# Optimization experiments

Measured on AMD Instinct MI355X. Metric: run time of the kernel, lower is better.

Reference implementation:

```python
import jax, jax.numpy as jnp
import numpy as np

BS = 128          # block_size for weight scales
FP8_MAX = 448.0   # e4m3fn max


def setup_inputs() -> dict:
    key = jax.random.key(0)
    k1, k2, k3 = jax.random.split(key, 3)
    T, I, O = 8192, 4096, 6144  # tokens, input_size, output_size
    x = jax.random.normal(k1, (T, I), dtype=jnp.float32)
    # weight is stored as fp8 in the module; we generate fp32 and cast inside reference
    weight = jax.random.normal(k2, (O, I), dtype=jnp.float32) * 0.02
    weight_scale_inv = jax.random.uniform(k3, (O // BS, I // BS), dtype=jnp.float32,
                                          minval=0.5, maxval=1.5)
    return {"x": x, "weight": weight, "weight_scale_inv": weight_scale_inv}


def reference(x, weight, weight_scale_inv):
    # --- stored fp8 weight (module keeps weight in float8_e4m3fn) ---
    w_fp8 = weight.astype(jnp.float8_e4m3fn)
    O, I = w_fp8.shape
    # --- block-wise dequantization: W_deq[o,i] = w[o,i] * scale[o//BS, i//BS] ---
    w_deq = (w_fp8.astype(jnp.float32)
             .reshape(O // BS, BS, I // BS, BS)
             * weight_scale_inv[:, None, :, None]).reshape(O, I)
    # --- dynamic per-token fp8 quantization of activations ---
    amax = jnp.clip(jnp.max(jnp.abs(x), axis=-1, keepdims=True), 1e-12, None)
    x_scale = (amax / FP8_MAX).astype(jnp.float32)   # [T, 1]
    x_fp8 = (x / x_scale).astype(jnp.float8_e4m3fn)  # [T, I]
    # --- GEMM on dequantized operands: out = (x_fp8 * x_scale) @ W_deq^T ---
    out = (x_fp8.astype(jnp.float32) @ w_deq.T) * x_scale  # [T, O]
    return out
```

## Files before the change

kernel.cpp:

```cpp
#include <hip/hip_runtime.h>
#include <hip/hip_bf16.h>
#include <stdint.h>

#define T_TOK 8192
#define K_IN  4096
#define O_OUT 6144

typedef __attribute__((ext_vector_type(4))) float f32x4;
typedef __attribute__((ext_vector_type(8))) int i32x8;
typedef unsigned int uint32;


__device__ inline void load_lds_16(const void* g, void* l) {
    __builtin_amdgcn_global_load_lds(
        (const __attribute__((address_space(1))) unsigned int*)g,
        (__attribute__((address_space(3))) unsigned int*)l, 16, 0, 0);
}

__device__ inline int pack4_fp8(float a, float b, float c, float d) {
    int r = __builtin_amdgcn_cvt_pk_fp8_f32(a, b, 0, false);
    r = __builtin_amdgcn_cvt_pk_fp8_f32(c, d, r, true);
    return r;
}

__global__ __launch_bounds__(256) void quant_x(const float* __restrict__ x,
                                               uint32* __restrict__ xq,
                                               float* __restrict__ xscale) {
    const int t   = blockIdx.x;
    const int tid = threadIdx.x;
    const float4* row4 = (const float4*)(x + (size_t)t * K_IN);

    float4 v[4];
    float amax = 0.f;
#pragma unroll
    for (int j = 0; j < 4; ++j) {
        v[j] = row4[tid + j * 256];
        amax = fmaxf(amax, fmaxf(fmaxf(fabsf(v[j].x), fabsf(v[j].y)),
                                 fmaxf(fabsf(v[j].z), fabsf(v[j].w))));
    }
#pragma unroll
    for (int off = 32; off > 0; off >>= 1)
        amax = fmaxf(amax, __shfl_down(amax, off, 64));
    __shared__ float red[4];
    if ((tid & 63) == 0) red[tid >> 6] = amax;
    __syncthreads();
    amax = fmaxf(fmaxf(red[0], red[1]), fmaxf(red[2], red[3]));

    const float scale = fmaxf(amax, 1e-12f) / 448.0f;
    if (tid == 0) xscale[t] = scale;

    uint32* orow = xq + (size_t)t * (K_IN / 4);
#pragma unroll
    for (int j = 0; j < 4; ++j) {
        float q0 = v[j].x / scale, q1 = v[j].y / scale;
        float q2 = v[j].z / scale, q3 = v[j].w / scale;
        orow[tid + j * 256] = (uint32)pack4_fp8(q0, q1, q2, q3);
    }
}

__global__ __launch_bounds__(256) void quant_w(const float* __restrict__ w,
                                               uint32* __restrict__ wq) {
    const size_t u = (size_t)blockIdx.x * 256 + threadIdx.x;
    float4 v = ((const float4*)w)[u];
    wq[u] = (uint32)pack4_fp8(v.x, v.y, v.z, v.w);
}

__global__ __launch_bounds__(256) void gemm_fp8(const unsigned char* __restrict__ A,
                                                const unsigned char* __restrict__ B,
                                                const float* __restrict__ sinv,
                                                const float* __restrict__ xscale,
                                                float* __restrict__ C) {
    constexpr int BM = 128, BN = 128, BK = 128;
    __shared__ unsigned char As[BM * BK];
    __shared__ unsigned char Bs[BN * BK];

    const int bn = blockIdx.x;
    const int bm = blockIdx.y;
    const int tid  = threadIdx.x;
    const int lane = tid & 63;
    const int wv   = tid >> 6;
    const int wm   = (wv >> 1) * 64;
    const int wn   = (wv & 1) * 64;

    const unsigned char* Abase = A + (size_t)(bm * BM) * K_IN;
    const unsigned char* Bbase = B + (size_t)(bn * BN) * K_IN;
    const float* srow = sinv + bn * (K_IN / 128);

    f32x4 acc[4][4] = {};
    float s_prev = srow[0];

    for (int kb = 0; kb < K_IN / BK; ++kb) {
        const int k0 = kb * BK;
#pragma unroll
        for (int s = 0; s < 4; ++s) {
            int c  = s * 256 + tid;
            int r  = c >> 3;
            int kc = (c & 7) ^ (r & 7);
            load_lds_16(Abase + (size_t)r * K_IN + k0 + kc * 16, &As[c * 16]);
        }
#pragma unroll
        for (int s = 0; s < 4; ++s) {
            int c  = s * 256 + tid;
            int r  = c >> 3;
            int kc = (c & 7) ^ (r & 7);
            load_lds_16(Bbase + (size_t)r * K_IN + k0 + kc * 16, &Bs[c * 16]);
        }
        __syncthreads();

        const float s_cur = srow[kb];
        const float rr = s_prev / s_cur;
        s_prev = s_cur;
#pragma unroll
        for (int i = 0; i < 4; ++i)
#pragma unroll
            for (int j = 0; j < 4; ++j)
                acc[i][j] = acc[i][j] * rr;

        union F { i32x8 v; int4 h[2]; } a[4], b[4];
        const int G2 = (lane >> 4) * 2;
#pragma unroll
        for (int i = 0; i < 4; ++i) {
            int r = wm + i * 16 + (lane & 15);
            a[i].h[0] = *(const int4*)&As[(r * 8 + (G2 ^ (r & 7))) * 16];
            a[i].h[1] = *(const int4*)&As[(r * 8 + ((G2 + 1) ^ (r & 7))) * 16];
        }
#pragma unroll
        for (int j = 0; j < 4; ++j) {
            int r = wn + j * 16 + (lane & 15);
            b[j].h[0] = *(const int4*)&Bs[(r * 8 + (G2 ^ (r & 7))) * 16];
            b[j].h[1] = *(const int4*)&Bs[(r * 8 + ((G2 + 1) ^ (r & 7))) * 16];
        }

#pragma unroll
        for (int i = 0; i < 4; ++i)
#pragma unroll
            for (int j = 0; j < 4; ++j)
                acc[i][j] = __builtin_amdgcn_mfma_scale_f32_16x16x128_f8f6f4(
                    a[i].v, b[j].v, acc[i][j],
                    0 , 0 ,
                    0, 0x7f7f7f7f,
                    0, 0x7f7f7f7f);
        __syncthreads();
    }

#pragma unroll
    for (int i = 0; i < 4; ++i) {
#pragma unroll
        for (int r = 0; r < 4; ++r) {
            int m_g = bm * BM + wm + i * 16 + (lane >> 4) * 4 + r;
            float f = xscale[m_g] * s_prev;
            float* crow = C + (size_t)m_g * O_OUT + bn * BN + wn;
#pragma unroll
            for (int j = 0; j < 4; ++j)
                crow[j * 16 + (lane & 15)] = acc[i][j][r] * f;
        }
    }
}

extern "C" void kernel_launch(void* const* d_in, const int* in_sizes, int n_in,
                              void* d_out, int out_size, void* d_ws, size_t ws_size,
                              hipStream_t stream) {
    const float* x    = (const float*)d_in[0];
    const float* w    = (const float*)d_in[1];
    const float* sinv = (const float*)d_in[2];
    float* out = (float*)d_out;

    char* ws = (char*)d_ws;
    uint32* xq = (uint32*)ws;
    uint32* wq = (uint32*)(ws + (size_t)T_TOK * K_IN);
    float* xscale = (float*)(ws + (size_t)T_TOK * K_IN
                                + (size_t)O_OUT * K_IN);

    quant_x<<<T_TOK, 256, 0, stream>>>(x, xq, xscale);
    quant_w<<<(O_OUT * K_IN) / (4 * 256), 256, 0, stream>>>(w, wq);
    dim3 grid(O_OUT / 128, T_TOK / 128);
    gemm_fp8<<<grid, 256, 0, stream>>>((const unsigned char*)xq,
                                       (const unsigned char*)wq,
                                       sinv, xscale, out);
}
```

Measured before the change: 639.9 us.

## Use 256x256 double-buffered LDS tiles with phased MFMA/load interleave

Rewrites the FP8 GEMM to use 256x256 output tiles with 512 threads (8 waves, each computing a 128x64 sub-tile), so each block does more math per byte loaded. It double-buffers the 128-byte K slices in 128KB of dynamic LDS, issuing the next tile's global-to-LDS copies while the current tile is computed. The MFMA work is split into four phases bracketed by barriers and s_setprio, so LDS fragment reads and accumulator rescaling interleave with matrix ops. The costs are heavy LDS use (one block per CU), many accumulator registers, and extra barriers inside each K step.

```diff
diff --git a/kernel.cpp b/kernel.cpp
--- a/kernel.cpp
+++ b/kernel.cpp
@@ -1,5 +1,4 @@
 #include <hip/hip_runtime.h>
-#include <hip/hip_bf16.h>
 #include <stdint.h>
 
 #define T_TOK 8192
@@ -65,96 +64,143 @@
     wq[u] = (uint32)pack4_fp8(v.x, v.y, v.z, v.w);
 }
 
-__global__ __launch_bounds__(256) void gemm_fp8(const unsigned char* __restrict__ A,
-                                                const unsigned char* __restrict__ B,
-                                                const float* __restrict__ sinv,
-                                                const float* __restrict__ xscale,
-                                                float* __restrict__ C) {
-    constexpr int BM = 128, BN = 128, BK = 128;
-    __shared__ unsigned char As[BM * BK];
-    __shared__ unsigned char Bs[BN * BK];
-
-    const int bn = blockIdx.x;
-    const int bm = blockIdx.y;
-    const int tid  = threadIdx.x;
+__global__ __launch_bounds__(512, 2) void gemm_fp8(const unsigned char* __restrict__ A,
+                                                   const unsigned char* __restrict__ B,
+                                                   const float* __restrict__ sinv,
+                                                   const float* __restrict__ xscale,
+                                                   float* __restrict__ C) {
+    constexpr int BM = 256, BN = 256, BK = 128;
+    constexpr int NKB = K_IN / BK;
+    extern __shared__ unsigned char smem[];
+
+    const int bn  = blockIdx.x;
+    const int bm  = blockIdx.y;
+    const int tid = threadIdx.x;
     const int lane = tid & 63;
     const int wv   = tid >> 6;
-    const int wm   = (wv >> 1) * 64;
-    const int wn   = (wv & 1) * 64;
-
-    const unsigned char* Abase = A + (size_t)(bm * BM) * K_IN;
-    const unsigned char* Bbase = B + (size_t)(bn * BN) * K_IN;
-    const float* srow = sinv + bn * (K_IN / 128);
-
-    f32x4 acc[4][4] = {};
+    const int wm   = (wv >> 2) * 128;
+    const int wn   = (wv & 3) * 64;
+    const int G2   = (lane >> 4) * 2;
+
+    const int tr = tid >> 3;
+    const int kc = (tid & 7) ^ (tr & 7);
+    const unsigned char* Ag = A + (size_t)(bm * BM + tr) * K_IN + kc * 16;
+    const unsigned char* Bg = B + (size_t)(bn * BN + tr) * K_IN + kc * 16;
+    const int ldst = tid * 16;
+
+    const int rA  = lane & 15;
+    const int sw  = lane & 7;
+    const int cs0 = ((G2    ) ^ sw) * 16;
+    const int cs1 = ((G2 | 1) ^ sw) * 16;
+
+    const float* srow = sinv + (size_t)(bn * 2 + (wn >> 7)) * NKB;
+
+    f32x4 acc[8][4] = {};
     float s_prev = srow[0];
 
-    for (int kb = 0; kb < K_IN / BK; ++kb) {
-        const int k0 = kb * BK;
-#pragma unroll
-        for (int s = 0; s < 4; ++s) {
-            int c  = s * 256 + tid;
-            int r  = c >> 3;
-            int kc = (c & 7) ^ (r & 7);
-            load_lds_16(Abase + (size_t)r * K_IN + k0 + kc * 16, &As[c * 16]);
-        }
-#pragma unroll
-        for (int s = 0; s < 4; ++s) {
-            int c  = s * 256 + tid;
-            int r  = c >> 3;
-            int kc = (c & 7) ^ (r & 7);
-            load_lds_16(Bbase + (size_t)r * K_IN + k0 + kc * 16, &Bs[c * 16]);
-        }
-        __syncthreads();
-
+#define STAGE_A(p_, k0_) {                                                   \
+    unsigned char* d_ = smem + (p_) * 65536 + ldst;                          \
+    _Pragma("unroll")                                                        \
+    for (int s_ = 0; s_ < 4; ++s_)                                           \
+        load_lds_16(Ag + (size_t)(s_ * 64) * K_IN + (k0_), d_ + s_ * 8192); }
+#define STAGE_B(p_, k0_) {                                                   \
+    unsigned char* d_ = smem + (p_) * 65536 + 32768 + ldst;                  \
+    _Pragma("unroll")                                                        \
+    for (int s_ = 0; s_ < 4; ++s_)                                           \
+        load_lds_16(Bg + (size_t)(s_ * 64) * K_IN + (k0_), d_ + s_ * 8192); }
+
+    union F { i32x8 v; int4 h[2]; };
+    F a[4], b01[2], b23[2];
+
+#define LDA(d_, i_) { const unsigned char* q_ = pA + (wm + (i_) * 16 + rA) * 128; \
+    (d_).h[0] = *(const int4*)(q_ + cs0); (d_).h[1] = *(const int4*)(q_ + cs1); }
+#define LDB(d_, j_) { const unsigned char* q_ = pB + (wn + (j_) * 16 + rA) * 128; \
+    (d_).h[0] = *(const int4*)(q_ + cs0); (d_).h[1] = *(const int4*)(q_ + cs1); }
+#define MFMA(i_, j_, af_, bf_)                                              \
+    acc[i_][j_] = __builtin_amdgcn_mfma_scale_f32_16x16x128_f8f6f4(         \
+        (af_).v, (bf_).v, acc[i_][j_], 0 , 0 ,            \
+        0, 0x7f7f7f7f, 0, 0x7f7f7f7f);
+#define WAIT_MFMA_PHASE() do {                                              \
+    asm volatile("" ::: "memory");                                          \
+    __builtin_amdgcn_s_barrier();                                           \
+    asm volatile("s_waitcnt lgkmcnt(0)" ::: "memory");                      \
+    __builtin_amdgcn_sched_barrier(0);                                      \
+    __builtin_amdgcn_s_setprio(1); } while (0)
+#define END_MFMA_PHASE() do {                                               \
+    __builtin_amdgcn_s_setprio(0);                                          \
+    asm volatile("" ::: "memory");                                          \
+    __builtin_amdgcn_s_barrier();                                           \
+    asm volatile("" ::: "memory"); } while (0)
+
+    STAGE_A(0, 0); STAGE_B(0, 0);
+    __syncthreads();
+
+    for (int kb = 0; kb < NKB; ++kb) {
+        const unsigned char* pA = smem + (kb & 1) * 65536;
+        const unsigned char* pB = pA + 32768;
+        const int  pn  = (kb & 1) ^ 1;
+        const int  nk0 = (kb + 1) * BK;
+        const bool pf  = (kb + 1) < NKB;
         const float s_cur = srow[kb];
         const float rr = s_prev / s_cur;
         s_prev = s_cur;
-#pragma unroll
-        for (int i = 0; i < 4; ++i)
-#pragma unroll
-            for (int j = 0; j < 4; ++j)
-                acc[i][j] = acc[i][j] * rr;
-
-        union F { i32x8 v; int4 h[2]; } a[4], b[4];
-        const int G2 = (lane >> 4) * 2;
-#pragma unroll
-        for (int i = 0; i < 4; ++i) {
-            int r = wm + i * 16 + (lane & 15);
-            a[i].h[0] = *(const int4*)&As[(r * 8 + (G2 ^ (r & 7))) * 16];
-            a[i].h[1] = *(const int4*)&As[(r * 8 + ((G2 + 1) ^ (r & 7))) * 16];
-        }
-#pragma unroll
-        for (int j = 0; j < 4; ++j) {
-            int r = wn + j * 16 + (lane & 15);
-            b[j].h[0] = *(const int4*)&Bs[(r * 8 + (G2 ^ (r & 7))) * 16];
-            b[j].h[1] = *(const int4*)&Bs[(r * 8 + ((G2 + 1) ^ (r & 7))) * 16];
-        }
-
-#pragma unroll
-        for (int i = 0; i < 4; ++i)
-#pragma unroll
-            for (int j = 0; j < 4; ++j)
-                acc[i][j] = __builtin_amdgcn_mfma_scale_f32_16x16x128_f8f6f4(
-                    a[i].v, b[j].v, acc[i][j],
-                    0 , 0 ,
-                    0, 0x7f7f7f7f,
-                    0, 0x7f7f7f7f);
+
+        if (pf) STAGE_A(pn, nk0);
+        LDA(a[0], 0) LDA(a[1], 1) LDA(a[2], 2) LDA(a[3], 3)
+        LDB(b01[0], 0) LDB(b01[1], 1)
+#pragma unroll
+        for (int i = 0; i < 4; ++i) { acc[i][0] *= rr; acc[i][1] *= rr; }
+        WAIT_MFMA_PHASE();
+#pragma unroll
+        for (int i = 0; i < 4; ++i) { MFMA(i, 0, a[i], b01[0]); MFMA(i, 1, a[i], b01[1]); }
+        END_MFMA_PHASE();
+
+        if (pf) STAGE_B(pn, nk0);
+        LDB(b23[0], 2) LDB(b23[1], 3)
+#pragma unroll
+        for (int i = 0; i < 4; ++i) { acc[i][2] *= rr; acc[i][3] *= rr; }
+        WAIT_MFMA_PHASE();
+#pragma unroll
+        for (int i = 0; i < 4; ++i) { MFMA(i, 2, a[i], b23[0]); MFMA(i, 3, a[i], b23[1]); }
+        END_MFMA_PHASE();
+
+        LDA(a[0], 4) LDA(a[1], 5) LDA(a[2], 6) LDA(a[3], 7)
+#pragma unroll
+        for (int i = 0; i < 4; ++i) { acc[4 + i][2] *= rr; acc[4 + i][3] *= rr; }
+        WAIT_MFMA_PHASE();
+#pragma unroll
+        for (int i = 0; i < 4; ++i) { MFMA(4 + i, 2, a[i], b23[0]); MFMA(4 + i, 3, a[i], b23[1]); }
+        END_MFMA_PHASE();
+
+        LDB(b01[0], 0) LDB(b01[1], 1)
+#pragma unroll
+        for (int i = 0; i < 4; ++i) { acc[4 + i][0] *= rr; acc[4 + i][1] *= rr; }
+        WAIT_MFMA_PHASE();
+#pragma unroll
+        for (int i = 0; i < 4; ++i) { MFMA(4 + i, 0, a[i], b01[0]); MFMA(4 + i, 1, a[i], b01[1]); }
+        __builtin_amdgcn_s_setprio(0);
         __syncthreads();
     }
 
 #pragma unroll
-    for (int i = 0; i < 4; ++i) {
+    for (int i = 0; i < 8; ++i) {
 #pragma unroll
         for (int r = 0; r < 4; ++r) {
-            int m_g = bm * BM + wm + i * 16 + (lane >> 4) * 4 + r;
-            float f = xscale[m_g] * s_prev;
+            const int m_g = bm * BM + wm + i * 16 + (lane >> 4) * 4 + r;
+            const float f = xscale[m_g] * s_prev;
             float* crow = C + (size_t)m_g * O_OUT + bn * BN + wn;
 #pragma unroll
             for (int j = 0; j < 4; ++j)
                 crow[j * 16 + (lane & 15)] = acc[i][j][r] * f;
         }
     }
+#undef STAGE_A
+#undef STAGE_B
+#undef LDA
+#undef LDB
+#undef MFMA
+#undef WAIT_MFMA_PHASE
+#undef END_MFMA_PHASE
 }
 
 extern "C" void kernel_launch(void* const* d_in, const int* in_sizes, int n_in,
@@ -173,8 +219,7 @@
 
     quant_x<<<T_TOK, 256, 0, stream>>>(x, xq, xscale);
     quant_w<<<(O_OUT * K_IN) / (4 * 256), 256, 0, stream>>>(w, wq);
-    dim3 grid(O_OUT / 128, T_TOK / 128);
-    gemm_fp8<<<grid, 256, 0, stream>>>((const unsigned char*)xq,
-                                       (const unsigned char*)wq,
-                                       sinv, xscale, out);
-}
+    dim3 grid(O_OUT / 256, T_TOK / 256);
+    gemm_fp8<<<grid, 512, 131072 , stream>>>(
+        (const unsigned char*)xq, (const unsigned char*)wq, sinv, xscale, out);
+}
```

After: 645.9 us. About the same (+0.9%).
